# Performance work log

Measured on AMD Instinct MI355X. Metric: run time of the kernel, lower is better.

## Reference

```python
import jax, jax.numpy as jnp
import numpy as np

B, S, K = 32, 256, 3   # batch, lattice length, max predecessors
D = 512                # dim_embedding == dim_rnn_input
H = 512                # dim_hidden
V = 50257              # vocab_size
L = 128                # label_vocab_size


def lattice_lstm(x, prev_idx, prev_w, Wih, Whh, bih, bhh):
    # x: [B,S,D]; prev_idx/prev_w: [B,S,K]; PyTorch LSTM gate layout (i,f,g,o).
    Bs, Sl, _ = x.shape
    Hh = Whh.shape[1]
    b_ar = jnp.arange(Bs)[:, None]  # [B,1] batch index for gather

    def step(carry, xs):
        hs, cs = carry              # stored per-timestep states [S,B,H]
        t, x_t, idx_t, w_t = xs     # [], [B,D], [B,K], [B,K]
        # weighted gather-pool over lattice predecessors; hs/cs are zero-init
        # so at t==0 this yields the zero initial state, as in the original.
        h = jnp.einsum('bk,bkh->bh', w_t, hs[idx_t, b_ar])
        c = jnp.einsum('bk,bkh->bh', w_t, cs[idx_t, b_ar])
        gates = x_t @ Wih.T + h @ Whh.T + (bih + bhh)  # [B,4H]
        i, f, g, o = jnp.split(gates, 4, axis=-1)
        c_new = jax.nn.sigmoid(f) * c + jax.nn.sigmoid(i) * jnp.tanh(g)
        h_new = jax.nn.sigmoid(o) * jnp.tanh(c_new)
        return (hs.at[t].set(h_new), cs.at[t].set(c_new)), h_new

    z = jnp.zeros((Sl, Bs, Hh), x.dtype)
    xs = (jnp.arange(Sl), x.swapaxes(0, 1), prev_idx.swapaxes(0, 1), prev_w.swapaxes(0, 1))
    _, outs = jax.lax.scan(step, (z, z), xs)
    return outs.swapaxes(0, 1)  # [B,S,H]


def _forward(inputs, positions, prev_idx, prev_w, emb, Wih, Whh, bih, bhh, W_lin, b_lin):
    x = emb[inputs]  # [B,S,D]
    out = lattice_lstm(x, prev_idx, prev_w, Wih, Whh, bih, bhh)
    # max-pool over the [start, end) span per batch element
    t_idx = jnp.arange(out.shape[1])[None, :]
    start, end = positions[:, 0:1], positions[:, 1:2]
    mask = (t_idx >= start) & (t_idx < end)                  # [B,S]
    pooled = jnp.where(mask[..., None], out, -1e30).max(axis=1)
    pooled = jnp.where(end > start, pooled, 0.0)             # empty span -> zeros
    return pooled @ W_lin.T + b_lin                          # [B,L]


def setup_inputs():
    key = jax.random.key(0)
    ks = jax.random.split(key, 12)
    inputs = jax.random.randint(ks[0], (B, S), 0, V)
    positions = jnp.concatenate([
        jax.random.randint(ks[1], (B, 1), 0, S // 2),
        jax.random.randint(ks[2], (B, 1), S // 2, S + 1)], axis=1)
    # predecessor indices must point strictly before t (DAG topological order)
    t = jnp.arange(S)[None, :, None]
    prev_idx = jax.random.randint(ks[3], (B, S, K), 0, S) % jnp.maximum(t, 1)
    u = jax.random.uniform(ks[4], (B, S, K)) + 0.1
    prev_w = u / u.sum(-1, keepdims=True)  # lattice marginals, sum to 1
    s = 1.0 / np.sqrt(H)
    emb = jax.random.uniform(ks[5], (V, D), minval=-0.1, maxval=0.1)
    Wih = jax.random.uniform(ks[6], (4 * H, D), minval=-s, maxval=s)
    Whh = jax.random.uniform(ks[7], (4 * H, H), minval=-s, maxval=s)
    bih = jax.random.uniform(ks[8], (4 * H,), minval=-s, maxval=s)
    bhh = jax.random.uniform(ks[9], (4 * H,), minval=-s, maxval=s)
    W_lin = jax.random.uniform(ks[10], (L, H), minval=-s, maxval=s)
    b_lin = jax.random.uniform(ks[11], (L,), minval=-s, maxval=s)
    return {"inputs": inputs, "positions": positions, "prev_idx": prev_idx,
            "prev_w": prev_w, "emb": emb, "Wih": Wih, "Whh": Whh,
            "bih": bih, "bhh": bhh, "W_lin": W_lin, "b_lin": b_lin}


def reference(inputs, positions, prev_idx, prev_w, emb, Wih, Whh, bih, bhh, W_lin, b_lin):
    return _forward(inputs, positions, prev_idx, prev_w, emb, Wih, Whh, bih, bhh, W_lin, b_lin)
```

## Files before the change

kernel.cpp:

```cpp
#include <hip/hip_runtime.h>


#define BB 32
#define SS 256
#define KKK 3
#define DD 512
#define HH 512
#define G4 2048
#define LL 128
#define NG 2
#define GS 8
#define NB 16
#define HSL 64

typedef __attribute__((ext_vector_type(4))) float f32x4;
typedef __attribute__((ext_vector_type(8))) short bf16x8;

__device__ __forceinline__ float blo(unsigned u){ return __builtin_bit_cast(float, u << 16); }
__device__ __forceinline__ float bhi(unsigned u){ return __builtin_bit_cast(float, u & 0xffff0000u); }
__device__ __forceinline__ unsigned f2bf(float f){
  unsigned x = __builtin_bit_cast(unsigned, f);
  x = x + 0x7fffu + ((x >> 16) & 1u);
  return x >> 16;
}
__device__ __forceinline__ float sigm(float x){ return 1.0f / (1.0f + __expf(-x)); }
__device__ __forceinline__ float tanh_(float x){
  float ax = fabsf(x);
  float e = __expf(-2.0f * ax);
  float r = (1.0f - e) / (1.0f + e);
  return x < 0.0f ? -r : r;
}
__device__ __forceinline__ void glds16(const void* g, void* lds){
  __builtin_amdgcn_global_load_lds((const __attribute__((address_space(1))) unsigned int*)g,
                                   (__attribute__((address_space(3))) unsigned int*)lds, 16, 0, 0);
}

__global__ __launch_bounds__(256) void prep_kernel(
    const int* __restrict__ inputs, const float* __restrict__ emb,
    const float* __restrict__ Wih, const float* __restrict__ bih, const float* __restrict__ bhh,
    unsigned short* __restrict__ Xb, unsigned short* __restrict__ Wihb, float* __restrict__ bias)
{
  int blk = blockIdx.x, tid = threadIdx.x;
  if (blk < 512){
    int row = blk * 16 + (tid >> 4);
    int d0 = (tid & 15) * 32;
    int b = row & 31, t = row >> 5;
    int tok = inputs[b * SS + t];
    const float* src = emb + (size_t)tok * DD + d0;
    unsigned short* dst = Xb + (size_t)row * DD + d0;
    #pragma unroll
    for (int j = 0; j < 32; j += 4){
      float4 v = *(const float4*)(src + j);
      uint2 o;
      o.x = f2bf(v.x) | (f2bf(v.y) << 16);
      o.y = f2bf(v.z) | (f2bf(v.w) << 16);
      *(uint2*)(dst + j) = o;
    }
  } else if (blk < 640){
    int row = (blk - 512) * 16 + (tid >> 4);
    int d0 = (tid & 15) * 32;
    const float* src = Wih + (size_t)row * DD + d0;
    unsigned short* dst = Wihb + (size_t)row * DD + d0;
    #pragma unroll
    for (int j = 0; j < 32; j += 4){
      float4 v = *(const float4*)(src + j);
      uint2 o;
      o.x = f2bf(v.x) | (f2bf(v.y) << 16);
      o.y = f2bf(v.z) | (f2bf(v.w) << 16);
      *(uint2*)(dst + j) = o;
    }
  } else {
    for (int n = tid; n < G4; n += 256) bias[n] = bih[n] + bhh[n];
  }
}

__global__ __launch_bounds__(256) void gemm_gx(
    const unsigned short* __restrict__ Xb, const unsigned short* __restrict__ Wihb,
    const float* __restrict__ bias, unsigned short* __restrict__ gx)
{
  __shared__ unsigned short As[128 * 32];
  __shared__ unsigned short Bs[128 * 32];
  const int tid = threadIdx.x;
  const int lane = tid & 63, wid = tid >> 6;
  const int m0 = blockIdx.x * 128, n0 = blockIdx.y * 128;
  const int wm = wid & 1, wn = wid >> 1;
  f32x4 acc[4][4];
  #pragma unroll
  for (int i = 0; i < 4; i++)
    #pragma unroll
    for (int j = 0; j < 4; j++)
      acc[i][j] = (f32x4){0.f, 0.f, 0.f, 0.f};

  for (int kk = 0; kk < DD; kk += 32){
    #pragma unroll
    for (int r = 0; r < 2; r++){
      int q = r * 256 + wid * 64 + lane;
      int row = q >> 2, seg = q & 3;
      glds16(Xb   + (size_t)(m0 + row) * DD + kk + seg * 8, As + (size_t)(r * 256 + wid * 64) * 8);
      glds16(Wihb + (size_t)(n0 + row) * DD + kk + seg * 8, Bs + (size_t)(r * 256 + wid * 64) * 8);
    }
    __syncthreads();
    bf16x8 af[4], bfv[4];
    #pragma unroll
    for (int i = 0; i < 4; i++){
      int ra = wm * 64 + i * 16 + (lane & 15);
      af[i] = *(const bf16x8*)(As + ra * 32 + (lane >> 4) * 8);
      int rb = wn * 64 + i * 16 + (lane & 15);
      bfv[i] = *(const bf16x8*)(Bs + rb * 32 + (lane >> 4) * 8);
    }
    #pragma unroll
    for (int i = 0; i < 4; i++)
      #pragma unroll
      for (int j = 0; j < 4; j++)
        acc[i][j] = __builtin_amdgcn_mfma_f32_16x16x32_bf16(af[i], bfv[j], acc[i][j], 0, 0, 0);
    __syncthreads();
  }
  #pragma unroll
  for (int j = 0; j < 4; j++){
    int ncol = n0 + wn * 64 + j * 16 + (lane & 15);
    float bv = bias[ncol];
    #pragma unroll
    for (int i = 0; i < 4; i++){
      int mbase = m0 + wm * 64 + i * 16 + (lane >> 4) * 4;
      #pragma unroll
      for (int r = 0; r < 4; r++)
        gx[(size_t)(mbase + r) * G4 + ncol] = (unsigned short)f2bf(acc[i][j][r] + bv);
    }
  }
}

__global__ __launch_bounds__(512, 1) void recur9(
    const int* __restrict__ prev_idx, const float* __restrict__ prev_w,
    const float* __restrict__ Whh, const int* __restrict__ positions,
    const unsigned short* __restrict__ gx,
    unsigned short* __restrict__ h_hist, float* __restrict__ c_hist,
    float* __restrict__ pooled, unsigned int* __restrict__ tags)
{
  __shared__ __align__(16) unsigned char hA[16 * 1024];
  __shared__ float gex[NB][264];
  __shared__ float wst2[2][NB * 3];
  __shared__ int   ist2[2][NB * 3];
  __shared__ int   wm_l[GS];
  __shared__ int   snap_l[GS];
  __shared__ int   mneed2[2];

  const int tid = threadIdx.x;
  const int lane = tid & 63, w = tid >> 6;
  const int bid = blockIdx.x, grp = bid >> 3, g = bid & 7;

  bf16x8 bfr0[16], bfr1[16];
  #pragma unroll
  for (int kf = 0; kf < 16; kf++){
    #pragma unroll
    for (int i = 0; i < 2; i++){
      int nt = 2 * w + i;
      int grow = (nt >> 2) * HH + g * HSL + ((nt & 3) << 4) + (lane & 15);
      int kcol = kf * 32 + ((lane >> 4) << 3);
      const float* p = Whh + (size_t)grow * HH + kcol;
      float4 v0 = *(const float4*)p;
      float4 v1 = *(const float4*)(p + 4);
      bf16x8 tf;
      tf[0] = (short)f2bf(v0.x); tf[1] = (short)f2bf(v0.y);
      tf[2] = (short)f2bf(v0.z); tf[3] = (short)f2bf(v0.w);
      tf[4] = (short)f2bf(v1.x); tf[5] = (short)f2bf(v1.y);
      tf[6] = (short)f2bf(v1.z); tf[7] = (short)f2bf(v1.w);
      if (i == 0) bfr0[kf] = tf; else bfr1[kf] = tf;
    }
  }

  const int cb = tid >> 5;
  const int jd = (tid & 31) << 1;
  const int bg = grp * NB + cb;
  const int gq = tid & 15;
  const int gd = tid >> 4;
  const int ggs = gd >> 2;
  const int gdof = (gd & 3) << 4;

  const int st = positions[bg * 2], en = positions[bg * 2 + 1];
  float pm0 = -1e30f, pm1 = -1e30f;
  const size_t cblk = (size_t)bid * ((size_t)SS * NB * HSL);
  const unsigned long long* hq = (const unsigned long long*)h_hist;
  unsigned* hbw = (unsigned*)h_hist;

  unsigned long long dq0[4], dq1[4], dq2[4];
  float2 cg0, cg1, cg2;
  unsigned gxv0, gxv1, gxv2, gxv3;

  if (tid < GS){ wm_l[tid] = 0; snap_l[tid] = 0; }
  __syncthreads();

  auto issue_gather = [&](int slot){
    int i0 = ist2[slot][gq * 3], i1 = ist2[slot][gq * 3 + 1], i2 = ist2[slot][gq * 3 + 2];
    size_t s0 = (((((size_t)i0 * NG + grp) * GS + ggs) * NB + gq) * HSL + gdof) >> 2;
    size_t s1 = (((((size_t)i1 * NG + grp) * GS + ggs) * NB + gq) * HSL + gdof) >> 2;
    size_t s2 = (((((size_t)i2 * NG + grp) * GS + ggs) * NB + gq) * HSL + gdof) >> 2;
    #pragma unroll
    for (int j = 0; j < 4; j++)
      dq0[j] = __hip_atomic_load(hq + s0 + j, __ATOMIC_RELAXED, __HIP_MEMORY_SCOPE_AGENT);
    #pragma unroll
    for (int j = 0; j < 4; j++)
      dq1[j] = __hip_atomic_load(hq + s1 + j, __ATOMIC_RELAXED, __HIP_MEMORY_SCOPE_AGENT);
    #pragma unroll
    for (int j = 0; j < 4; j++)
      dq2[j] = __hip_atomic_load(hq + s2 + j, __ATOMIC_RELAXED, __HIP_MEMORY_SCOPE_AGENT);
  };
  auto issue_cgx = [&](int slot, int tn){
    const float* cb0 = c_hist + cblk + (size_t)cb * HSL + jd;
    cg0 = *(const float2*)(cb0 + (size_t)ist2[slot][cb * 3]     * (NB * HSL));
    cg1 = *(const float2*)(cb0 + (size_t)ist2[slot][cb * 3 + 1] * (NB * HSL));
    cg2 = *(const float2*)(cb0 + (size_t)ist2[slot][cb * 3 + 2] * (NB * HSL));
    const unsigned short* gxr = gx + ((size_t)tn * BB + bg) * G4 + g * HSL + jd;
    gxv0 = *(const unsigned*)(gxr);
    gxv1 = *(const unsigned*)(gxr + 512);
    gxv2 = *(const unsigned*)(gxr + 1024);
    gxv3 = *(const unsigned*)(gxr + 1536);
  };

  {
    const unsigned short* gxr = gx + (size_t)bg * G4 + g * HSL + jd;
    gxv0 = *(const unsigned*)(gxr);
    gxv1 = *(const unsigned*)(gxr + 512);
    gxv2 = *(const unsigned*)(gxr + 1024);
    gxv3 = *(const unsigned*)(gxr + 1536);
    int iv = -1;
    if (tid < NB * 3){
      int b = tid / 3, k = tid - b * 3;
      iv = prev_idx[(size_t)(grp * NB + b) * (SS * KKK) + 1 * KKK + k];
      ist2[1][tid] = iv;
      wst2[1][tid] = prev_w[(size_t)(grp * NB + b) * (SS * KKK) + 1 * KKK + k];
    }
    if (tid < 64){
      int m = iv;
      #pragma unroll
      for (int off = 32; off; off >>= 1) m = max(m, __shfl_xor(m, off));
      if (tid == 0) mneed2[1] = m;
    }
    float cn0 = sigm(blo(gxv0)) * tanh_(blo(gxv2));
    float cn1 = sigm(bhi(gxv0)) * tanh_(bhi(gxv2));
    float hn0 = sigm(blo(gxv3)) * tanh_(cn0);
    float hn1 = sigm(bhi(gxv3)) * tanh_(cn1);
    *(float2*)(c_hist + cblk + (size_t)cb * HSL + jd) = make_float2(cn0, cn1);
    unsigned hv = f2bf(hn0) | (f2bf(hn1) << 16);
    __hip_atomic_store(hbw + (((((size_t)grp * GS + g) * NB + cb) * HSL + jd) >> 1), hv,
                       __ATOMIC_RELAXED, __HIP_MEMORY_SCOPE_AGENT);
    if (0 >= st && 0 < en){ pm0 = fmaxf(pm0, hn0); pm1 = fmaxf(pm1, hn1); }
    __syncthreads();
    if (tid == 0){
      __hip_atomic_store(&tags[grp * GS + g], 1u, __ATOMIC_RELAXED, __HIP_MEMORY_SCOPE_AGENT);
      wm_l[g] = 1;
    }
    issue_cgx(1, 1);
  }
  bool valid = false;

  for (int t = 1; t < SS; t++){
    const int sl = t & 1, sn = sl ^ 1;

    unsigned tsnap = 0;
    if (tid < GS)
      tsnap = __hip_atomic_load(&tags[grp * GS + tid], __ATOMIC_RELAXED,
                                __HIP_MEMORY_SCOPE_AGENT);

    if (!valid){
      const int need = mneed2[sl] + 1;
      if (tid < GS && tid != g){
        int v = wm_l[tid];
        if (v < need){
          const unsigned int* tp = tags + grp * GS + tid;
          do {
            v = (int)__hip_atomic_load(tp, __ATOMIC_RELAXED, __HIP_MEMORY_SCOPE_AGENT);
            if (v < need) __builtin_amdgcn_s_sleep(1);
          } while (v < need);
          wm_l[tid] = v;
        }
      }
      __syncthreads();
      issue_gather(sl);
    }

    {
      float w0 = wst2[sl][gq * 3], w1 = wst2[sl][gq * 3 + 1], w2 = wst2[sl][gq * 3 + 2];
      unsigned pk[8];
      #pragma unroll
      for (int j = 0; j < 4; j++){
        unsigned a_lo = (unsigned)dq0[j], a_hi = (unsigned)(dq0[j] >> 32);
        unsigned b_lo = (unsigned)dq1[j], b_hi = (unsigned)(dq1[j] >> 32);
        unsigned c_lo = (unsigned)dq2[j], c_hi = (unsigned)(dq2[j] >> 32);
        float l0 = w0 * blo(a_lo) + w1 * blo(b_lo) + w2 * blo(c_lo);
        float h0 = w0 * bhi(a_lo) + w1 * bhi(b_lo) + w2 * bhi(c_lo);
        float l1 = w0 * blo(a_hi) + w1 * blo(b_hi) + w2 * blo(c_hi);
        float h1 = w0 * bhi(a_hi) + w1 * bhi(b_hi) + w2 * bhi(c_hi);
        pk[2 * j]     = f2bf(l0) | (f2bf(h0) << 16);
        pk[2 * j + 1] = f2bf(l1) | (f2bf(h1) << 16);
      }
      int ob = (gq << 10) + gd * 32;
      int xr = (gq & 7) << 4;
      *(uint4*)(hA + (ob ^ xr))        = (uint4){pk[0], pk[1], pk[2], pk[3]};
      *(uint4*)(hA + ((ob + 16) ^ xr)) = (uint4){pk[4], pk[5], pk[6], pk[7]};
    }
    __syncthreads();

    int iv = -1;
    if (t + 1 < SS){
      if (tid < NB * 3){
        int b = tid / 3, k = tid - b * 3;
        iv = prev_idx[(size_t)(grp * NB + b) * (SS * KKK) + (t + 1) * KKK + k];
        ist2[sn][tid] = iv;
        wst2[sn][tid] = prev_w[(size_t)(grp * NB + b) * (SS * KKK) + (t + 1) * KKK + k];
      }
    }
    {
      f32x4 p00 = {0,0,0,0}, p01 = {0,0,0,0}, p10 = {0,0,0,0}, p11 = {0,0,0,0};
      const int rA = lane & 15;
      const int kb = (lane >> 4) << 4;
      const int xr = (rA & 7) << 4;
      const int rbase = rA << 10;
      #pragma unroll
      for (int kf = 0; kf < 16; kf += 2){
        bf16x8 a0 = *(const bf16x8*)(hA + ((rbase + kf * 64 + kb) ^ xr));
        bf16x8 a1 = *(const bf16x8*)(hA + ((rbase + (kf + 1) * 64 + kb) ^ xr));
        p00 = __builtin_amdgcn_mfma_f32_16x16x32_bf16(a0, bfr0[kf],     p00, 0, 0, 0);
        p10 = __builtin_amdgcn_mfma_f32_16x16x32_bf16(a0, bfr1[kf],     p10, 0, 0, 0);
        p01 = __builtin_amdgcn_mfma_f32_16x16x32_bf16(a1, bfr0[kf + 1], p01, 0, 0, 0);
        p11 = __builtin_amdgcn_mfma_f32_16x16x32_bf16(a1, bfr1[kf + 1], p11, 0, 0, 0);
      }
      int cl0 = (2 * w) * 16 + rA, cl1 = cl0 + 16;
      #pragma unroll
      for (int j = 0; j < 4; j++){
        int bq = ((lane >> 4) << 2) + j;
        gex[bq][cl0] = p00[j] + p01[j];
        gex[bq][cl1] = p10[j] + p11[j];
      }
    }
    if (t + 1 < SS && tid < 64){
      int m = iv;
      #pragma unroll
      for (int off = 32; off; off >>= 1) m = max(m, __shfl_xor(m, off));
      if (tid == 0) mneed2[sn] = m;
    }
    if (tid < GS) snap_l[tid] = (int)tsnap;
    __syncthreads();

    bool validn = false;
    if (t + 1 < SS){
      const int need = mneed2[sn] + 1;
      int m = max(wm_l[0], snap_l[0]);
      #pragma unroll
      for (int p = 1; p < GS; p++) m = min(m, max(wm_l[p], snap_l[p]));
      validn = (m >= need);
      if (validn) issue_gather(sn);
    }

    {
      float w0 = wst2[sl][cb * 3], w1 = wst2[sl][cb * 3 + 1], w2 = wst2[sl][cb * 3 + 2];
      float g_i0 = blo(gxv0) + gex[cb][jd];
      float g_i1 = bhi(gxv0) + gex[cb][jd + 1];
      float g_f0 = blo(gxv1) + gex[cb][64 + jd];
      float g_f1 = bhi(gxv1) + gex[cb][64 + jd + 1];
      float g_g0 = blo(gxv2) + gex[cb][128 + jd];
      float g_g1 = bhi(gxv2) + gex[cb][128 + jd + 1];
      float g_o0 = blo(gxv3) + gex[cb][192 + jd];
      float g_o1 = bhi(gxv3) + gex[cb][192 + jd + 1];
      float co0 = w0 * cg0.x + w1 * cg1.x + w2 * cg2.x;
      float co1 = w0 * cg0.y + w1 * cg1.y + w2 * cg2.y;
      float cn0 = sigm(g_f0) * co0 + sigm(g_i0) * tanh_(g_g0);
      float cn1 = sigm(g_f1) * co1 + sigm(g_i1) * tanh_(g_g1);
      float hn0 = sigm(g_o0) * tanh_(cn0);
      float hn1 = sigm(g_o1) * tanh_(cn1);
      *(float2*)(c_hist + cblk + ((size_t)t * NB + cb) * HSL + jd) = make_float2(cn0, cn1);
      unsigned hv = f2bf(hn0) | (f2bf(hn1) << 16);
      __hip_atomic_store(hbw + ((((((size_t)t * NG + grp) * GS + g) * NB + cb) * HSL + jd) >> 1),
                         hv, __ATOMIC_RELAXED, __HIP_MEMORY_SCOPE_AGENT);
      if (t >= st && t < en){ pm0 = fmaxf(pm0, hn0); pm1 = fmaxf(pm1, hn1); }
    }
    if (tid < GS) wm_l[tid] = max(wm_l[tid], snap_l[tid]);
    __syncthreads();

    if (tid == 0)
      __hip_atomic_store(&tags[grp * GS + g], (unsigned)(t + 1),
                         __ATOMIC_RELAXED, __HIP_MEMORY_SCOPE_AGENT);
    if (t + 1 < SS)
      issue_cgx(sn, t + 1);
    valid = validn;
  }

  pooled[(size_t)bg * HH + g * HSL + jd]     = (en > st && pm0 > -1e29f) ? pm0 : 0.f;
  pooled[(size_t)bg * HH + g * HSL + jd + 1] = (en > st && pm1 > -1e29f) ? pm1 : 0.f;
}

__global__ __launch_bounds__(128) void pool_lin(
    const float* __restrict__ pooled, const float* __restrict__ W_lin,
    const float* __restrict__ b_lin, float* __restrict__ out)
{
  __shared__ float p[HH];
  int b = blockIdx.x, tid = threadIdx.x;
  *(float4*)&p[tid * 4] = *(const float4*)&pooled[(size_t)b * HH + tid * 4];
  __syncthreads();
  float acc = b_lin[tid];
  const float* wr = W_lin + (size_t)tid * HH;
  #pragma unroll 8
  for (int h = 0; h < HH; h += 4){
    float4 w = *(const float4*)(wr + h);
    acc += w.x * p[h] + w.y * p[h+1] + w.z * p[h+2] + w.w * p[h+3];
  }
  out[b * LL + tid] = acc;
}

extern "C" void kernel_launch(void* const* d_in, const int* in_sizes, int n_in,
                              void* d_out, int out_size, void* d_ws, size_t ws_size,
                              hipStream_t stream)
{
  (void)in_sizes; (void)n_in; (void)out_size; (void)ws_size;
  const int*   inputs    = (const int*)  d_in[0];
  const int*   positions = (const int*)  d_in[1];
  const int*   prev_idx  = (const int*)  d_in[2];
  const float* prev_w    = (const float*)d_in[3];
  const float* emb       = (const float*)d_in[4];
  const float* Wih       = (const float*)d_in[5];
  const float* Whh       = (const float*)d_in[6];
  const float* bih       = (const float*)d_in[7];
  const float* bhh       = (const float*)d_in[8];
  const float* W_lin     = (const float*)d_in[9];
  const float* b_lin     = (const float*)d_in[10];
  float* out = (float*)d_out;
  char* ws = (char*)d_ws;

  unsigned int*   tags   = (unsigned int*)  ws;
  unsigned short* Xb     = (unsigned short*)(ws + 4096);
  unsigned short* Wihb   = (unsigned short*)(ws + 8392704);
  float*          bias   = (float*)         (ws + 10489856);
  unsigned short* gx     = (unsigned short*)(ws + 10498048);
  unsigned short* h_hist = (unsigned short*)(ws + 44052480);
  float*          c_hist = (float*)         (ws + 52441088);
  float*          pooled = (float*)         (ws + 69218304);

  hipMemsetAsync(tags, 0, 4096, stream);
  prep_kernel<<<641, 256, 0, stream>>>(inputs, emb, Wih, bih, bhh, Xb, Wihb, bias);
  gemm_gx<<<dim3(64, 16), 256, 0, stream>>>(Xb, Wihb, bias, gx);
  recur9<<<16, 512, 0, stream>>>(prev_idx, prev_w, Whh, positions, gx, h_hist, c_hist, pooled, tags);
  pool_lin<<<32, 128, 0, stream>>>(pooled, W_lin, b_lin, out);
}
```

Before: 1.455 ms.

## Replace shared-memory watermark tracking with per-wave registers and trim block barriers

Every wave now keeps its own copy of the cross-block progress watermarks in a lane register and reduces them with wave shuffles, so the shared-memory watermark and snapshot arrays are gone. This removes one __syncthreads in the spin-wait path and one at the end of each step. The prefetch gather for the next step moves after the gate computation and is followed by an inline-asm waitcnt plus s_barrier. The cost is redundant polling by every wave and a hand-written waitcnt count (vmcnt 12) that assumes a particular number of outstanding loads, which is fragile if the compiler reorders memory operations.

```diff
diff --git a/kernel.cpp b/kernel.cpp
--- a/kernel.cpp
+++ b/kernel.cpp
@@ -129,7 +129,7 @@
   }
 }
 
-__global__ __launch_bounds__(512, 1) void recur9(
+__global__ __launch_bounds__(512, 1) void recur10(
     const int* __restrict__ prev_idx, const float* __restrict__ prev_w,
     const float* __restrict__ Whh, const int* __restrict__ positions,
     const unsigned short* __restrict__ gx,
@@ -140,8 +140,6 @@
   __shared__ float gex[NB][264];
   __shared__ float wst2[2][NB * 3];
   __shared__ int   ist2[2][NB * 3];
-  __shared__ int   wm_l[GS];
-  __shared__ int   snap_l[GS];
   __shared__ int   mneed2[2];
 
   const int tid = threadIdx.x;
@@ -186,8 +184,7 @@
   float2 cg0, cg1, cg2;
   unsigned gxv0, gxv1, gxv2, gxv3;
 
-  if (tid < GS){ wm_l[tid] = 0; snap_l[tid] = 0; }
-  __syncthreads();
+  int wmr = (lane == g) ? 0 : 0;
 
   auto issue_gather = [&](int slot){
     int i0 = ist2[slot][gq * 3], i1 = ist2[slot][gq * 3 + 1], i2 = ist2[slot][gq * 3 + 2];
@@ -245,10 +242,9 @@
                        __ATOMIC_RELAXED, __HIP_MEMORY_SCOPE_AGENT);
     if (0 >= st && 0 < en){ pm0 = fmaxf(pm0, hn0); pm1 = fmaxf(pm1, hn1); }
     __syncthreads();
-    if (tid == 0){
+    if (tid == 0)
       __hip_atomic_store(&tags[grp * GS + g], 1u, __ATOMIC_RELAXED, __HIP_MEMORY_SCOPE_AGENT);
-      wm_l[g] = 1;
-    }
+    if (lane == g) wmr = 1;
     issue_cgx(1, 1);
   }
   bool valid = false;
@@ -257,24 +253,23 @@
     const int sl = t & 1, sn = sl ^ 1;
 
     unsigned tsnap = 0;
-    if (tid < GS)
-      tsnap = __hip_atomic_load(&tags[grp * GS + tid], __ATOMIC_RELAXED,
+    if (lane < GS)
+      tsnap = __hip_atomic_load(&tags[grp * GS + lane], __ATOMIC_RELAXED,
                                 __HIP_MEMORY_SCOPE_AGENT);
 
     if (!valid){
       const int need = mneed2[sl] + 1;
-      if (tid < GS && tid != g){
-        int v = wm_l[tid];
+      if (lane < GS){
+        int v = wmr;
         if (v < need){
-          const unsigned int* tp = tags + grp * GS + tid;
+          const unsigned int* tp = tags + grp * GS + lane;
           do {
             v = (int)__hip_atomic_load(tp, __ATOMIC_RELAXED, __HIP_MEMORY_SCOPE_AGENT);
             if (v < need) __builtin_amdgcn_s_sleep(1);
           } while (v < need);
-          wm_l[tid] = v;
+          wmr = v;
         }
       }
-      __syncthreads();
       issue_gather(sl);
     }
 
@@ -338,18 +333,7 @@
       for (int off = 32; off; off >>= 1) m = max(m, __shfl_xor(m, off));
       if (tid == 0) mneed2[sn] = m;
     }
-    if (tid < GS) snap_l[tid] = (int)tsnap;
     __syncthreads();
-
-    bool validn = false;
-    if (t + 1 < SS){
-      const int need = mneed2[sn] + 1;
-      int m = max(wm_l[0], snap_l[0]);
-      #pragma unroll
-      for (int p = 1; p < GS; p++) m = min(m, max(wm_l[p], snap_l[p]));
-      validn = (m >= need);
-      if (validn) issue_gather(sn);
-    }
 
     {
       float w0 = wst2[sl][cb * 3], w1 = wst2[sl][cb * 3 + 1], w2 = wst2[sl][cb * 3 + 2];
@@ -373,12 +357,32 @@
                          hv, __ATOMIC_RELAXED, __HIP_MEMORY_SCOPE_AGENT);
       if (t >= st && t < en){ pm0 = fmaxf(pm0, hn0); pm1 = fmaxf(pm1, hn1); }
     }
-    if (tid < GS) wm_l[tid] = max(wm_l[tid], snap_l[tid]);
-    __syncthreads();
+    asm volatile("" ::: "memory");
+    __builtin_amdgcn_sched_barrier(0);
+
+    if (lane < GS) wmr = max(wmr, (int)tsnap);
+    bool validn = false;
+    if (t + 1 < SS){
+      int vm = (lane < GS) ? wmr : 0x7fffffff;
+      vm = min(vm, __shfl_xor(vm, 1));
+      vm = min(vm, __shfl_xor(vm, 2));
+      vm = min(vm, __shfl_xor(vm, 4));
+      int m = __shfl(vm, 0);
+      validn = (m >= mneed2[sn] + 1);
+    }
+    if (validn){
+      issue_gather(sn);
+      asm volatile("s_waitcnt vmcnt(12) lgkmcnt(0)\n\ts_barrier" ::: "memory");
+      __builtin_amdgcn_sched_barrier(0);
+    } else {
+      asm volatile("s_waitcnt vmcnt(0) lgkmcnt(0)\n\ts_barrier" ::: "memory");
+      __builtin_amdgcn_sched_barrier(0);
+    }
 
     if (tid == 0)
       __hip_atomic_store(&tags[grp * GS + g], (unsigned)(t + 1),
                          __ATOMIC_RELAXED, __HIP_MEMORY_SCOPE_AGENT);
+    if (lane == g) wmr = max(wmr, t + 1);
     if (t + 1 < SS)
       issue_cgx(sn, t + 1);
     valid = validn;
@@ -437,6 +441,6 @@
   hipMemsetAsync(tags, 0, 4096, stream);
   prep_kernel<<<641, 256, 0, stream>>>(inputs, emb, Wih, bih, bhh, Xb, Wihb, bias);
   gemm_gx<<<dim3(64, 16), 256, 0, stream>>>(Xb, Wihb, bias, gx);
-  recur9<<<16, 512, 0, stream>>>(prev_idx, prev_w, Whh, positions, gx, h_hist, c_hist, pooled, tags);
+  recur10<<<16, 512, 0, stream>>>(prev_idx, prev_w, Whh, positions, gx, h_hist, c_hist, pooled, tags);
   pool_lin<<<32, 128, 0, stream>>>(pooled, W_lin, b_lin, out);
 }
```

New measurement: 1.545 ms. +6.1%, slower.
